# Kernel tuning notes

Measured on AMD Instinct MI355X. Metric: run time of the kernel, lower is better.

## Reference

```python
import jax, jax.numpy as jnp
import numpy as np

# bin sizes: logspace(-3,0,20) seconds, keep those < (t_end - t_start)/2 = 0.25 s, in ms
_bs = np.logspace(-3, 0, 20)
BIN_MS = [int(b) for b in np.round(_bs[_bs < 0.25] * 1000).astype(int)]  # 16 bins: [1,1,2,3,4,6,9,13,18,26,38,55,78,113,162,234]

SYNC_COST = 10.0
T_START_MS, T_END_MS = 0, 500
EPS = 1e-7


def setup_inputs() -> dict:
    C, B, T, N, N_E = 50, 8, 600, 30000, 24000
    rng = np.random.default_rng(42)
    spikes = (rng.random((B, T, N)) < 0.02).astype(np.float32)
    sample_trials = rng.integers(0, B, size=C).astype(np.int32)
    # sample_counts ~ N(70, 30) clipped to [15, N_E], consecutive chunks of a shuffled e-id list
    counts = np.clip(rng.normal(70.0, 30.0, C).astype(np.int64), 15, N_E)
    e_ids = rng.permutation(N_E)
    sel_mask = np.zeros((C, N), dtype=bool)
    prev = 0
    for i in range(C):
        cn = int(counts[i])
        if prev + cn > N_E:
            e_ids = rng.permutation(e_ids)
            prev = 0
        sel_mask[i, e_ids[prev:prev + cn]] = True
        prev += cn
    exp_fanos = (rng.random(len(BIN_MS)) * 1.5 + 0.5).astype(np.float32)
    return {
        "spikes": jnp.asarray(spikes),
        "exp_fanos": jnp.asarray(exp_fanos),
        "sample_trials": jnp.asarray(sample_trials),
        "sel_mask": jnp.asarray(sel_mask),
    }


def reference(spikes, exp_fanos, sample_trials, sel_mask):
    # trim to analysis window: [B, 500, N]
    sp = spikes[:, T_START_MS:T_END_MS, :]
    C = sel_mask.shape[0]
    m = sel_mask.astype(sp.dtype)  # [C, N]
    # population spike count per sample: sum over selected e-cells.
    # M[b, t, c] = sum_n sp[b,t,n] * m[c,n]; then pick the sampled trial per c.
    M = jnp.einsum('btn,cn->btc', sp, m)                 # [B, T, C] (small)
    selected = M[sample_trials, :, jnp.arange(C)]        # [C, T]
    T = selected.shape[1]
    fanos = []
    for b in BIN_MS:  # fixed small set of bin sizes
        nb = T // b
        # conv1d(ones, stride=b, VALID) == non-overlapping binned sums
        counts = selected[:, :nb * b].reshape(C, nb, b).sum(axis=-1)  # [C, nb]
        mean_count = jnp.maximum(counts.mean(axis=1), EPS)
        var_count = counts.var(axis=1)  # population variance, matches tf.math.reduce_variance
        fanos.append(jnp.mean(var_count / mean_count))
    fanos = jnp.stack(fanos)  # [16]
    mse_loss = jnp.mean(jnp.square(exp_fanos - fanos))
    return SYNC_COST * mse_loss
```

## Files before the change

### kernel.cpp

```cpp
#include <hip/hip_runtime.h>

#define C_CLS 50
#define B_TR 8
#define T_FULL 600
#define T_USE 500
#define N_NEU 30000
#define NGRP 118
#define NGRP_PAD 120
#define WPC 480
#define NQ 30
#define TPB 4
#define NBINS 16
#define EPS 1e-7
#define LDS_STRIDE 501

__device__ __constant__ int d_bins[NBINS] = {1,1,2,3,4,6,9,13,18,26,38,55,78,113,162,234};


__device__ __forceinline__ int mode_from_verdict(int v) {
    if (v & 1) return 2;
    if (v & 8) return 4;
    if (v & 2) return 1;
    if (v & 4) return 0;
    return 3;
}

__device__ __forceinline__ bool load_sel(const void* mask, int mode, long long e) {
    switch (mode) {
        case 0:  return ((const int*)mask)[e] != 0;
        case 1:  return ((const unsigned char*)mask)[e] != 0;
        case 2:  return ((const float*)mask)[e] != 0.0f;
        case 3:  return ((const long long*)mask)[e] != 0LL;
        default: return ((const double*)mask)[e] != 0.0;
    }
}

__global__ void __launch_bounds__(256)
detect_kernel(const unsigned int* __restrict__ w, const int* __restrict__ trials,
              int* verdict, int* ncls, int* cls_of_trial) {
    __shared__ int sfl;
    if (threadIdx.x == 0) sfl = 0;
    __syncthreads();
    const int nwords = C_CLS * N_NEU / 4;
    int per = (nwords + gridDim.x - 1) / gridDim.x;
    int beg = blockIdx.x * per;
    int end = beg + per; if (end > nwords) end = nwords;
    int f = 0;
    for (int i = beg + threadIdx.x; i < end; i += blockDim.x) {
        unsigned int v = w[i];
        if (v == 0u) continue;
        if (v == 0x3F800000u) f |= 1;
        else if (v == 0x3FF00000u && (i & 1)) f |= 8;
        else {
            unsigned int b0 = v & 0xFFu, b1 = (v >> 8) & 0xFFu,
                         b2 = (v >> 16) & 0xFFu, b3 = (v >> 24) & 0xFFu;
            bool byteOK = (b0 <= 1u) && (b1 <= 1u) && (b2 <= 1u) && (b3 <= 1u);
            if (byteOK && v != 1u) f |= 2;
        }
        if (i & 1) f |= 4;
    }
    if (f) atomicOr(&sfl, f);
    __syncthreads();
    if (threadIdx.x == 0) verdict[blockIdx.x] = sfl;

    if (blockIdx.x == 0 && threadIdx.x < 64) {
        int lane = threadIdx.x;
        int b = (lane < C_CLS) ? trials[lane] : -1;
        for (int bb = 0; bb < B_TR; ++bb) {
            unsigned long long m = __ballot(b == bb);
            if (b == bb) {
                int pos = __popcll(m & ((1ull << lane) - 1ull));
                cls_of_trial[bb * 64 + pos] = lane;
            }
            if (lane == 0) ncls[bb] = __popcll(m);
        }
    }
}

__global__ void build_bits_kernel(const void* mask, const int* __restrict__ verdict,
                                  unsigned long long* bits) {
    int c = blockIdx.x;
    int lane = threadIdx.x;
    int v = verdict[lane] | verdict[lane + 64] | verdict[lane + 128] | verdict[lane + 192];
    for (int off = 32; off > 0; off >>= 1) v |= __shfl_xor(v, off);
    int mode = mode_from_verdict(v);
    for (int g = blockIdx.y; g < NGRP_PAD; g += gridDim.y) {
        int base = g * 256 + lane * 4;
        long long e = (long long)c * N_NEU + base;
        bool s0 = (base + 0 < N_NEU) && load_sel(mask, mode, e + 0);
        bool s1 = (base + 1 < N_NEU) && load_sel(mask, mode, e + 1);
        bool s2 = (base + 2 < N_NEU) && load_sel(mask, mode, e + 2);
        bool s3 = (base + 3 < N_NEU) && load_sel(mask, mode, e + 3);
        unsigned long long w0 = __ballot(s0);
        unsigned long long w1 = __ballot(s1);
        unsigned long long w2 = __ballot(s2);
        unsigned long long w3 = __ballot(s3);
        if (lane == 0) {
            long long o = (long long)c * WPC + g * 4;
            bits[o + 0] = w0; bits[o + 1] = w1;
            bits[o + 2] = w2; bits[o + 3] = w3;
        }
    }
}

__global__ void __launch_bounds__(256)
stream_kernel(const float* __restrict__ spikes,
              const int* __restrict__ ncls,
              const int* __restrict__ cls_of_trial,
              const unsigned long long* __restrict__ bits,
              float* __restrict__ selected) {
    __shared__ unsigned long long sbits[TPB][WPC];
    __shared__ int wsum2[C_CLS][4][2];
    int bt = blockIdx.x;
    int b = bt / (T_USE / TPB);
    int tq = bt - b * (T_USE / TPB);
    int t0 = tq * TPB;
    int nc = ncls[b];
    if (nc == 0) return;
    int lane = threadIdx.x & 63;
    int wid = threadIdx.x >> 6;
    const float4* __restrict__ row4 =
        (const float4*)(spikes + ((long long)(b * T_FULL + t0 + wid)) * N_NEU);

    for (int q = 0; q < NQ; ++q) {
        float4 v[4];
#pragma unroll
        for (int u = 0; u < 4; ++u) {
            int ia = (q * 4 + u) * 64 + lane;
            if (ia > N_NEU / 4 - 1) ia = N_NEU / 4 - 1;
            v[u] = row4[ia];
        }
#pragma unroll
        for (int u = 0; u < 4; ++u) {
            unsigned long long b0 = __ballot(v[u].x != 0.0f);
            unsigned long long b1 = __ballot(v[u].y != 0.0f);
            unsigned long long b2 = __ballot(v[u].z != 0.0f);
            unsigned long long b3 = __ballot(v[u].w != 0.0f);
            if (lane == 0) {
                int o = (q * 4 + u) * 4;
                sbits[wid][o + 0] = b0; sbits[wid][o + 1] = b1;
                sbits[wid][o + 2] = b2; sbits[wid][o + 3] = b3;
            }
        }
    }
    __syncthreads();

    int i0 = threadIdx.x;
    int i1 = threadIdx.x + 256;
    bool has1 = (i1 < WPC);
    unsigned long long s00 = sbits[0][i0], s10 = sbits[1][i0],
                       s20 = sbits[2][i0], s30 = sbits[3][i0];
    unsigned long long s01 = 0, s11 = 0, s21 = 0, s31 = 0;
    if (has1) { s01 = sbits[0][i1]; s11 = sbits[1][i1];
                s21 = sbits[2][i1]; s31 = sbits[3][i1]; }
    for (int kc = 0; kc < nc; ++kc) {
        int c = cls_of_trial[b * 64 + kc];
        const unsigned long long* __restrict__ bp = bits + (long long)c * WPC;
        unsigned long long w0 = bp[i0];
        unsigned long long w1 = has1 ? bp[i1] : 0ull;
        int p0 = __popcll(s00 & w0) + __popcll(s01 & w1);
        int p1 = __popcll(s10 & w0) + __popcll(s11 & w1);
        int p2 = __popcll(s20 & w0) + __popcll(s21 & w1);
        int p3 = __popcll(s30 & w0) + __popcll(s31 & w1);
        int pa = p0 | (p1 << 16);
        int pb = p2 | (p3 << 16);
        for (int off = 32; off > 0; off >>= 1) {
            pa += __shfl_down(pa, off);
            pb += __shfl_down(pb, off);
        }
        if (lane == 0) { wsum2[kc][wid][0] = pa; wsum2[kc][wid][1] = pb; }
    }
    __syncthreads();
    if (threadIdx.x < nc * 4) {
        int kc = threadIdx.x >> 2, r = threadIdx.x & 3;
        int c = cls_of_trial[b * 64 + kc];
        int s = 0;
#pragma unroll
        for (int w = 0; w < 4; ++w) {
            int v = wsum2[kc][w][r >> 1];
            s += (r & 1) ? (v >> 16) : (v & 0xFFFF);
        }
        selected[c * T_USE + t0 + r] = (float)s;
    }
}

__global__ void __launch_bounds__(1024)
fano_loss_kernel(const float* __restrict__ selected,
                 const float* __restrict__ exp_fanos,
                 float* __restrict__ out) {
    __shared__ float lds[C_CLS * LDS_STRIDE];
    __shared__ float sf[NBINS];
    const float4* __restrict__ sel4 = (const float4*)selected;
    for (int i = threadIdx.x; i < C_CLS * T_USE / 4; i += 1024) {
        float4 v = sel4[i];
        int r = i / (T_USE / 4);
        int p = (i - r * (T_USE / 4)) * 4;
        float* dst = &lds[r * LDS_STRIDE + p];
        dst[0] = v.x; dst[1] = v.y; dst[2] = v.z; dst[3] = v.w;
    }
    __syncthreads();
    int wid = threadIdx.x >> 6;
    int lane = threadIdx.x & 63;
    int b = d_bins[wid];
    int nb = T_USE / b;
    float fano = 0.f;
    if (lane < C_CLS) {
        const float* row = &lds[lane * LDS_STRIDE];
        double s1 = 0.0, s2 = 0.0;
        for (int i = 0; i < nb; ++i) {
            float cs = 0.f;
            int base = i * b;
            for (int j = 0; j < b; ++j) cs += row[base + j];
            s1 += cs;
            s2 += (double)cs * (double)cs;
        }
        double mean = s1 / nb;
        double var = s2 / nb - mean * mean;
        if (var < 0.0) var = 0.0;
        double m = mean > EPS ? mean : EPS;
        fano = (float)(var / m);
    }
    for (int off = 32; off > 0; off >>= 1) fano += __shfl_down(fano, off);
    if (lane == 0) sf[wid] = fano / (float)C_CLS;
    __syncthreads();
    if (wid == 0) {
        float sq = 0.f;
        if (lane < NBINS) {
            float d = exp_fanos[lane] - sf[lane];
            sq = d * d;
        }
        for (int off = 32; off > 0; off >>= 1) sq += __shfl_down(sq, off);
        if (lane == 0) out[0] = 10.0f * sq / (float)NBINS;
    }
}

extern "C" void kernel_launch(void* const* d_in, const int* in_sizes, int n_in,
                              void* d_out, int out_size, void* d_ws, size_t ws_size,
                              hipStream_t stream) {
    const float* spikes    = (const float*)d_in[0];
    const float* exp_fanos = (const float*)d_in[1];
    const int*   trials    = (const int*)d_in[2];
    const void*  mask      = d_in[3];
    float* out = (float*)d_out;

    char* ws = (char*)d_ws;
    int*   verdict = (int*)(ws + 0);
    int*   ncls    = (int*)(ws + 1024);
    int*   clsofb  = (int*)(ws + 1280);
    unsigned long long* bits = (unsigned long long*)(ws + 8192);
    float* selected = (float*)(ws + 204800);

    detect_kernel<<<256, 256, 0, stream>>>((const unsigned int*)mask, trials,
                                           verdict, ncls, clsofb);
    build_bits_kernel<<<dim3(C_CLS, 8), 64, 0, stream>>>(mask, verdict, bits);
    stream_kernel<<<B_TR * (T_USE / TPB), 256, 0, stream>>>(spikes, ncls, clsofb,
                                                            bits, selected);
    fano_loss_kernel<<<1, 1024, 0, stream>>>(selected, exp_fanos, out);
}
```

Before: 181.3 us.

## Fuse four kernels into one cooperative persistent kernel with grid syncs

Replaces the detect, bit-build, streaming and fano kernels with one cooperative kernel of 512 blocks that separates phases with grid.sync. This removes three kernel launch gaps and the serial single-block fano stage. The fano stage is now split across 16 blocks, one per bin size, each reading rows straight from global memory instead of staging them in LDS. The cost is grid-wide barriers, a persistent loop over 1000 stream tiles in 512 blocks, and less parallelism in the bit-build phase.

```diff
diff --git a/kernel.cpp b/kernel.cpp
--- a/kernel.cpp
+++ b/kernel.cpp
@@ -1,4 +1,7 @@
 #include <hip/hip_runtime.h>
+#include <hip/hip_cooperative_groups.h>
+
+namespace cg = cooperative_groups;
 
 #define C_CLS 50
 #define B_TR 8
@@ -10,12 +13,12 @@
 #define WPC 480
 #define NQ 30
 #define TPB 4
+#define NBT (B_TR * T_USE / TPB)
+#define GRID 512
 #define NBINS 16
 #define EPS 1e-7
-#define LDS_STRIDE 501
 
 __device__ __constant__ int d_bins[NBINS] = {1,1,2,3,4,6,9,13,18,26,38,55,78,113,162,234};
-
 
 __device__ __forceinline__ int mode_from_verdict(int v) {
     if (v & 1) return 2;
@@ -35,198 +38,199 @@
     }
 }
 
-__global__ void __launch_bounds__(256)
-detect_kernel(const unsigned int* __restrict__ w, const int* __restrict__ trials,
-              int* verdict, int* ncls, int* cls_of_trial) {
-    __shared__ int sfl;
-    if (threadIdx.x == 0) sfl = 0;
-    __syncthreads();
-    const int nwords = C_CLS * N_NEU / 4;
-    int per = (nwords + gridDim.x - 1) / gridDim.x;
-    int beg = blockIdx.x * per;
-    int end = beg + per; if (end > nwords) end = nwords;
-    int f = 0;
-    for (int i = beg + threadIdx.x; i < end; i += blockDim.x) {
-        unsigned int v = w[i];
-        if (v == 0u) continue;
-        if (v == 0x3F800000u) f |= 1;
-        else if (v == 0x3FF00000u && (i & 1)) f |= 8;
-        else {
-            unsigned int b0 = v & 0xFFu, b1 = (v >> 8) & 0xFFu,
-                         b2 = (v >> 16) & 0xFFu, b3 = (v >> 24) & 0xFFu;
-            bool byteOK = (b0 <= 1u) && (b1 <= 1u) && (b2 <= 1u) && (b3 <= 1u);
-            if (byteOK && v != 1u) f |= 2;
-        }
-        if (i & 1) f |= 4;
-    }
-    if (f) atomicOr(&sfl, f);
-    __syncthreads();
-    if (threadIdx.x == 0) verdict[blockIdx.x] = sfl;
-
-    if (blockIdx.x == 0 && threadIdx.x < 64) {
-        int lane = threadIdx.x;
-        int b = (lane < C_CLS) ? trials[lane] : -1;
-        for (int bb = 0; bb < B_TR; ++bb) {
-            unsigned long long m = __ballot(b == bb);
-            if (b == bb) {
-                int pos = __popcll(m & ((1ull << lane) - 1ull));
-                cls_of_trial[bb * 64 + pos] = lane;
-            }
-            if (lane == 0) ncls[bb] = __popcll(m);
-        }
-    }
-}
-
-__global__ void build_bits_kernel(const void* mask, const int* __restrict__ verdict,
-                                  unsigned long long* bits) {
-    int c = blockIdx.x;
-    int lane = threadIdx.x;
-    int v = verdict[lane] | verdict[lane + 64] | verdict[lane + 128] | verdict[lane + 192];
-    for (int off = 32; off > 0; off >>= 1) v |= __shfl_xor(v, off);
-    int mode = mode_from_verdict(v);
-    for (int g = blockIdx.y; g < NGRP_PAD; g += gridDim.y) {
-        int base = g * 256 + lane * 4;
-        long long e = (long long)c * N_NEU + base;
-        bool s0 = (base + 0 < N_NEU) && load_sel(mask, mode, e + 0);
-        bool s1 = (base + 1 < N_NEU) && load_sel(mask, mode, e + 1);
-        bool s2 = (base + 2 < N_NEU) && load_sel(mask, mode, e + 2);
-        bool s3 = (base + 3 < N_NEU) && load_sel(mask, mode, e + 3);
-        unsigned long long w0 = __ballot(s0);
-        unsigned long long w1 = __ballot(s1);
-        unsigned long long w2 = __ballot(s2);
-        unsigned long long w3 = __ballot(s3);
-        if (lane == 0) {
-            long long o = (long long)c * WPC + g * 4;
-            bits[o + 0] = w0; bits[o + 1] = w1;
-            bits[o + 2] = w2; bits[o + 3] = w3;
-        }
-    }
-}
-
-__global__ void __launch_bounds__(256)
-stream_kernel(const float* __restrict__ spikes,
-              const int* __restrict__ ncls,
-              const int* __restrict__ cls_of_trial,
-              const unsigned long long* __restrict__ bits,
-              float* __restrict__ selected) {
+__global__ void __launch_bounds__(256, 2)
+fused_kernel(const float* __restrict__ spikes,
+             const float* __restrict__ exp_fanos,
+             const int* __restrict__ trials,
+             const void* __restrict__ mask,
+             float* __restrict__ out,
+             int* __restrict__ verdict,
+             int* __restrict__ ncls,
+             int* __restrict__ cls_of_trial,
+             unsigned long long* __restrict__ bits,
+             float* __restrict__ selected,
+             float* __restrict__ fanos) {
+    cg::grid_group grid = cg::this_grid();
     __shared__ unsigned long long sbits[TPB][WPC];
     __shared__ int wsum2[C_CLS][4][2];
-    int bt = blockIdx.x;
-    int b = bt / (T_USE / TPB);
-    int tq = bt - b * (T_USE / TPB);
-    int t0 = tq * TPB;
-    int nc = ncls[b];
-    if (nc == 0) return;
-    int lane = threadIdx.x & 63;
-    int wid = threadIdx.x >> 6;
-    const float4* __restrict__ row4 =
-        (const float4*)(spikes + ((long long)(b * T_FULL + t0 + wid)) * N_NEU);
-
-    for (int q = 0; q < NQ; ++q) {
-        float4 v[4];
-#pragma unroll
-        for (int u = 0; u < 4; ++u) {
-            int ia = (q * 4 + u) * 64 + lane;
-            if (ia > N_NEU / 4 - 1) ia = N_NEU / 4 - 1;
-            v[u] = row4[ia];
-        }
-#pragma unroll
-        for (int u = 0; u < 4; ++u) {
-            unsigned long long b0 = __ballot(v[u].x != 0.0f);
-            unsigned long long b1 = __ballot(v[u].y != 0.0f);
-            unsigned long long b2 = __ballot(v[u].z != 0.0f);
-            unsigned long long b3 = __ballot(v[u].w != 0.0f);
-            if (lane == 0) {
-                int o = (q * 4 + u) * 4;
-                sbits[wid][o + 0] = b0; sbits[wid][o + 1] = b1;
-                sbits[wid][o + 2] = b2; sbits[wid][o + 3] = b3;
-            }
-        }
-    }
-    __syncthreads();
-
-    int i0 = threadIdx.x;
-    int i1 = threadIdx.x + 256;
-    bool has1 = (i1 < WPC);
-    unsigned long long s00 = sbits[0][i0], s10 = sbits[1][i0],
-                       s20 = sbits[2][i0], s30 = sbits[3][i0];
-    unsigned long long s01 = 0, s11 = 0, s21 = 0, s31 = 0;
-    if (has1) { s01 = sbits[0][i1]; s11 = sbits[1][i1];
-                s21 = sbits[2][i1]; s31 = sbits[3][i1]; }
-    for (int kc = 0; kc < nc; ++kc) {
-        int c = cls_of_trial[b * 64 + kc];
-        const unsigned long long* __restrict__ bp = bits + (long long)c * WPC;
-        unsigned long long w0 = bp[i0];
-        unsigned long long w1 = has1 ? bp[i1] : 0ull;
-        int p0 = __popcll(s00 & w0) + __popcll(s01 & w1);
-        int p1 = __popcll(s10 & w0) + __popcll(s11 & w1);
-        int p2 = __popcll(s20 & w0) + __popcll(s21 & w1);
-        int p3 = __popcll(s30 & w0) + __popcll(s31 & w1);
-        int pa = p0 | (p1 << 16);
-        int pb = p2 | (p3 << 16);
-        for (int off = 32; off > 0; off >>= 1) {
-            pa += __shfl_down(pa, off);
-            pb += __shfl_down(pb, off);
-        }
-        if (lane == 0) { wsum2[kc][wid][0] = pa; wsum2[kc][wid][1] = pb; }
-    }
-    __syncthreads();
-    if (threadIdx.x < nc * 4) {
-        int kc = threadIdx.x >> 2, r = threadIdx.x & 3;
-        int c = cls_of_trial[b * 64 + kc];
-        int s = 0;
-#pragma unroll
-        for (int w = 0; w < 4; ++w) {
-            int v = wsum2[kc][w][r >> 1];
-            s += (r & 1) ? (v >> 16) : (v & 0xFFFF);
-        }
-        selected[c * T_USE + t0 + r] = (float)s;
-    }
-}
-
-__global__ void __launch_bounds__(1024)
-fano_loss_kernel(const float* __restrict__ selected,
-                 const float* __restrict__ exp_fanos,
-                 float* __restrict__ out) {
-    __shared__ float lds[C_CLS * LDS_STRIDE];
-    __shared__ float sf[NBINS];
-    const float4* __restrict__ sel4 = (const float4*)selected;
-    for (int i = threadIdx.x; i < C_CLS * T_USE / 4; i += 1024) {
-        float4 v = sel4[i];
-        int r = i / (T_USE / 4);
-        int p = (i - r * (T_USE / 4)) * 4;
-        float* dst = &lds[r * LDS_STRIDE + p];
-        dst[0] = v.x; dst[1] = v.y; dst[2] = v.z; dst[3] = v.w;
-    }
-    __syncthreads();
-    int wid = threadIdx.x >> 6;
-    int lane = threadIdx.x & 63;
-    int b = d_bins[wid];
-    int nb = T_USE / b;
-    float fano = 0.f;
-    if (lane < C_CLS) {
-        const float* row = &lds[lane * LDS_STRIDE];
-        double s1 = 0.0, s2 = 0.0;
-        for (int i = 0; i < nb; ++i) {
+    __shared__ int sfl;
+
+    const int bid = blockIdx.x;
+    const int tid = threadIdx.x;
+    const int lane = tid & 63;
+    const int wid = tid >> 6;
+
+    {
+        if (tid == 0) sfl = 0;
+        __syncthreads();
+        const unsigned int* w = (const unsigned int*)mask;
+        const int nwords = C_CLS * N_NEU / 4;
+        int f = 0;
+        for (int i = bid * 256 + tid; i < nwords; i += GRID * 256) {
+            unsigned int v = w[i];
+            if (v == 0u) continue;
+            if (v == 0x3F800000u) f |= 1;
+            else if (v == 0x3FF00000u && (i & 1)) f |= 8;
+            else {
+                unsigned int b0 = v & 0xFFu, b1 = (v >> 8) & 0xFFu,
+                             b2 = (v >> 16) & 0xFFu, b3 = (v >> 24) & 0xFFu;
+                bool byteOK = (b0 <= 1u) && (b1 <= 1u) && (b2 <= 1u) && (b3 <= 1u);
+                if (byteOK && v != 1u) f |= 2;
+            }
+            if (i & 1) f |= 4;
+        }
+        for (int off = 32; off > 0; off >>= 1) f |= __shfl_xor(f, off);
+        if (lane == 0 && f) atomicOr(&sfl, f);
+        __syncthreads();
+        if (tid == 0) verdict[bid] = sfl;
+
+        if (bid == 0 && tid < 64) {
+            int b = (lane < C_CLS) ? trials[lane] : -1;
+            for (int bb = 0; bb < B_TR; ++bb) {
+                unsigned long long m = __ballot(b == bb);
+                if (b == bb) {
+                    int pos = __popcll(m & ((1ull << lane) - 1ull));
+                    cls_of_trial[bb * 64 + pos] = lane;
+                }
+                if (lane == 0) ncls[bb] = __popcll(m);
+            }
+        }
+    }
+    __threadfence();
+    grid.sync();
+
+    {
+        if (tid == 0) sfl = 0;
+        __syncthreads();
+        int v = verdict[tid] | verdict[tid + 256];
+        for (int off = 32; off > 0; off >>= 1) v |= __shfl_xor(v, off);
+        if (lane == 0 && v) atomicOr(&sfl, v);
+        __syncthreads();
+        int mode = mode_from_verdict(sfl);
+        for (int task = bid; task < C_CLS * NGRP_PAD; task += GRID) {
+            int c = task / NGRP_PAD;
+            int g = task - c * NGRP_PAD;
+            int n = g * 256 + lane * 4 + wid;
+            bool sel = (n < N_NEU) && load_sel(mask, mode, (long long)c * N_NEU + n);
+            unsigned long long w = __ballot(sel);
+            if (lane == 0) bits[(long long)c * WPC + g * 4 + wid] = w;
+        }
+    }
+    __threadfence();
+    grid.sync();
+
+    for (int bt = bid; bt < NBT; bt += GRID) {
+        int b = bt / (T_USE / TPB);
+        int tq = bt - b * (T_USE / TPB);
+        int t0 = tq * TPB;
+        int nc = ncls[b];
+        if (nc == 0) continue;
+        const float4* __restrict__ row4 =
+            (const float4*)(spikes + ((long long)(b * T_FULL + t0 + wid)) * N_NEU);
+
+        for (int q = 0; q < NQ; ++q) {
+            float4 v[4];
+#pragma unroll
+            for (int u = 0; u < 4; ++u) {
+                int ia = (q * 4 + u) * 64 + lane;
+                if (ia > N_NEU / 4 - 1) ia = N_NEU / 4 - 1;
+                v[u] = row4[ia];
+            }
+#pragma unroll
+            for (int u = 0; u < 4; ++u) {
+                unsigned long long b0 = __ballot(v[u].x != 0.0f);
+                unsigned long long b1 = __ballot(v[u].y != 0.0f);
+                unsigned long long b2 = __ballot(v[u].z != 0.0f);
+                unsigned long long b3 = __ballot(v[u].w != 0.0f);
+                if (lane == 0) {
+                    int o = (q * 4 + u) * 4;
+                    sbits[wid][o + 0] = b0; sbits[wid][o + 1] = b1;
+                    sbits[wid][o + 2] = b2; sbits[wid][o + 3] = b3;
+                }
+            }
+        }
+        __syncthreads();
+
+        int i0 = tid;
+        int i1 = tid + 256;
+        bool has1 = (i1 < WPC);
+        unsigned long long s00 = sbits[0][i0], s10 = sbits[1][i0],
+                           s20 = sbits[2][i0], s30 = sbits[3][i0];
+        unsigned long long s01 = 0, s11 = 0, s21 = 0, s31 = 0;
+        if (has1) { s01 = sbits[0][i1]; s11 = sbits[1][i1];
+                    s21 = sbits[2][i1]; s31 = sbits[3][i1]; }
+        for (int kc = 0; kc < nc; ++kc) {
+            int c = cls_of_trial[b * 64 + kc];
+            const unsigned long long* __restrict__ bp = bits + (long long)c * WPC;
+            unsigned long long w0 = bp[i0];
+            unsigned long long w1 = has1 ? bp[i1] : 0ull;
+            int p0 = __popcll(s00 & w0) + __popcll(s01 & w1);
+            int p1 = __popcll(s10 & w0) + __popcll(s11 & w1);
+            int p2 = __popcll(s20 & w0) + __popcll(s21 & w1);
+            int p3 = __popcll(s30 & w0) + __popcll(s31 & w1);
+            int pa = p0 | (p1 << 16);
+            int pb = p2 | (p3 << 16);
+            for (int off = 32; off > 0; off >>= 1) {
+                pa += __shfl_down(pa, off);
+                pb += __shfl_down(pb, off);
+            }
+            if (lane == 0) { wsum2[kc][wid][0] = pa; wsum2[kc][wid][1] = pb; }
+        }
+        __syncthreads();
+        if (tid < nc * 4) {
+            int kc = tid >> 2, r = tid & 3;
+            int c = cls_of_trial[b * 64 + kc];
+            int s = 0;
+#pragma unroll
+            for (int w = 0; w < 4; ++w) {
+                int v = wsum2[kc][w][r >> 1];
+                s += (r & 1) ? (v >> 16) : (v & 0xFFFF);
+            }
+            selected[c * T_USE + t0 + r] = (float)s;
+        }
+    }
+    __threadfence();
+    grid.sync();
+
+    if (bid < NBINS && tid < 64) {
+        int b = d_bins[bid];
+        int nb = T_USE / b;
+        int lim = nb * b;
+        float fano = 0.f;
+        if (lane < C_CLS) {
+            const float4* __restrict__ row4 = (const float4*)(selected + lane * T_USE);
+            double s1 = 0.0, s2 = 0.0;
             float cs = 0.f;
-            int base = i * b;
-            for (int j = 0; j < b; ++j) cs += row[base + j];
-            s1 += cs;
-            s2 += (double)cs * (double)cs;
-        }
-        double mean = s1 / nb;
-        double var = s2 / nb - mean * mean;
-        if (var < 0.0) var = 0.0;
-        double m = mean > EPS ? mean : EPS;
-        fano = (float)(var / m);
-    }
-    for (int off = 32; off > 0; off >>= 1) fano += __shfl_down(fano, off);
-    if (lane == 0) sf[wid] = fano / (float)C_CLS;
-    __syncthreads();
-    if (wid == 0) {
+            int r = b;
+            for (int i4 = 0; i4 < T_USE / 4; ++i4) {
+                float4 v = row4[i4];
+                float comp0 = v.x, comp1 = v.y, comp2 = v.z, comp3 = v.w;
+#pragma unroll
+                for (int u = 0; u < 4; ++u) {
+                    float cv = (u == 0) ? comp0 : (u == 1) ? comp1 : (u == 2) ? comp2 : comp3;
+                    int idx = i4 * 4 + u;
+                    if (idx < lim) {
+                        cs += cv;
+                        if (--r == 0) { s1 += cs; s2 += (double)cs * cs; cs = 0.f; r = b; }
+                    }
+                }
+            }
+            double mean = s1 / nb;
+            double var = s2 / nb - mean * mean;
+            if (var < 0.0) var = 0.0;
+            double m = mean > EPS ? mean : EPS;
+            fano = (float)(var / m);
+        }
+        for (int off = 32; off > 0; off >>= 1) fano += __shfl_down(fano, off);
+        if (lane == 0) fanos[bid] = fano / (float)C_CLS;
+    }
+    __threadfence();
+    grid.sync();
+
+    if (bid == 0 && tid < 64) {
         float sq = 0.f;
         if (lane < NBINS) {
-            float d = exp_fanos[lane] - sf[lane];
+            float d = exp_fanos[lane] - fanos[lane];
             sq = d * d;
         }
         for (int off = 32; off > 0; off >>= 1) sq += __shfl_down(sq, off);
@@ -245,15 +249,17 @@
 
     char* ws = (char*)d_ws;
     int*   verdict = (int*)(ws + 0);
-    int*   ncls    = (int*)(ws + 1024);
-    int*   clsofb  = (int*)(ws + 1280);
+    int*   ncls    = (int*)(ws + 2048);
+    int*   clsofb  = (int*)(ws + 2304);
+    float* fanos   = (float*)(ws + 4608);
     unsigned long long* bits = (unsigned long long*)(ws + 8192);
     float* selected = (float*)(ws + 204800);
 
-    detect_kernel<<<256, 256, 0, stream>>>((const unsigned int*)mask, trials,
-                                           verdict, ncls, clsofb);
-    build_bits_kernel<<<dim3(C_CLS, 8), 64, 0, stream>>>(mask, verdict, bits);
-    stream_kernel<<<B_TR * (T_USE / TPB), 256, 0, stream>>>(spikes, ncls, clsofb,
-                                                            bits, selected);
-    fano_loss_kernel<<<1, 1024, 0, stream>>>(selected, exp_fanos, out);
-}
+    void* args[] = {
+        (void*)&spikes, (void*)&exp_fanos, (void*)&trials, (void*)&mask,
+        (void*)&out, (void*)&verdict, (void*)&ncls, (void*)&clsofb,
+        (void*)&bits, (void*)&selected, (void*)&fanos
+    };
+    hipLaunchCooperativeKernel((void*)fused_kernel, dim3(GRID), dim3(256),
+                               args, 0, stream);
+}
```

Result: slower. 483.3 us (+166.6%).

## Split spike rows across two waves per timestep and software-pipeline loads

Applied to the files above, without the earlier changes.

The stream kernel now handles 2 timesteps per block instead of 4, with two waves splitting each 30000-neuron row in half. This doubles the block count for more parallelism. Each wave double-buffers its float4 loads so the next chunk's global reads are issued before the ballots on the current one. The bitmask words are padded to 512 per class, which removes the tail guards, and launch bounds ask for 4 blocks per CU. The risks are extra register pressure from the prefetch buffers and the need for build_bits and the bits workspace to agree with the new 512-word padding.

```diff
diff --git a/kernel.cpp b/kernel.cpp
--- a/kernel.cpp
+++ b/kernel.cpp
@@ -5,11 +5,12 @@
 #define T_FULL 600
 #define T_USE 500
 #define N_NEU 30000
-#define NGRP 118
-#define NGRP_PAD 120
-#define WPC 480
-#define NQ 30
-#define TPB 4
+#define NF4 7500
+#define NGRP_PAD 128
+#define WPC 512
+#define NQHALF 16
+#define TPB 2
+#define NBT (B_TR * T_USE / TPB)
 #define NBINS 16
 #define EPS 1e-7
 #define LDS_STRIDE 501
@@ -103,14 +104,40 @@
     }
 }
 
-__global__ void __launch_bounds__(256)
+__device__ __forceinline__ void loadq(float4* v, const float4* __restrict__ row4,
+                                      int qq, int lane) {
+#pragma unroll
+    for (int u = 0; u < 4; ++u) {
+        int ia = (qq * 4 + u) * 64 + lane;
+        if (ia > NF4 - 1) ia = NF4 - 1;
+        v[u] = row4[ia];
+    }
+}
+
+__device__ __forceinline__ void consumeq(const float4* v, unsigned long long* sb,
+                                         int qq, int lane) {
+#pragma unroll
+    for (int u = 0; u < 4; ++u) {
+        unsigned long long b0 = __ballot(v[u].x != 0.0f);
+        unsigned long long b1 = __ballot(v[u].y != 0.0f);
+        unsigned long long b2 = __ballot(v[u].z != 0.0f);
+        unsigned long long b3 = __ballot(v[u].w != 0.0f);
+        if (lane == 0) {
+            int o = (qq * 4 + u) * 4;
+            sb[o + 0] = b0; sb[o + 1] = b1;
+            sb[o + 2] = b2; sb[o + 3] = b3;
+        }
+    }
+}
+
+__global__ void __launch_bounds__(256, 4)
 stream_kernel(const float* __restrict__ spikes,
               const int* __restrict__ ncls,
               const int* __restrict__ cls_of_trial,
               const unsigned long long* __restrict__ bits,
               float* __restrict__ selected) {
     __shared__ unsigned long long sbits[TPB][WPC];
-    __shared__ int wsum2[C_CLS][4][2];
+    __shared__ int wsum[C_CLS][4];
     int bt = blockIdx.x;
     int b = bt / (T_USE / TPB);
     int tq = bt - b * (T_USE / TPB);
@@ -119,68 +146,56 @@
     if (nc == 0) return;
     int lane = threadIdx.x & 63;
     int wid = threadIdx.x >> 6;
+    int r = wid >> 1;
+    int h = wid & 1;
     const float4* __restrict__ row4 =
-        (const float4*)(spikes + ((long long)(b * T_FULL + t0 + wid)) * N_NEU);
-
-    for (int q = 0; q < NQ; ++q) {
-        float4 v[4];
-#pragma unroll
-        for (int u = 0; u < 4; ++u) {
-            int ia = (q * 4 + u) * 64 + lane;
-            if (ia > N_NEU / 4 - 1) ia = N_NEU / 4 - 1;
-            v[u] = row4[ia];
-        }
-#pragma unroll
-        for (int u = 0; u < 4; ++u) {
-            unsigned long long b0 = __ballot(v[u].x != 0.0f);
-            unsigned long long b1 = __ballot(v[u].y != 0.0f);
-            unsigned long long b2 = __ballot(v[u].z != 0.0f);
-            unsigned long long b3 = __ballot(v[u].w != 0.0f);
-            if (lane == 0) {
-                int o = (q * 4 + u) * 4;
-                sbits[wid][o + 0] = b0; sbits[wid][o + 1] = b1;
-                sbits[wid][o + 2] = b2; sbits[wid][o + 3] = b3;
-            }
+        (const float4*)(spikes + ((long long)(b * T_FULL + t0 + r)) * N_NEU);
+
+    int qb = h * NQHALF;
+    float4 A[4], B[4], NA[4], NB[4];
+    loadq(A, row4, qb + 0, lane);
+    loadq(B, row4, qb + 1, lane);
+    for (int q = 0; q < NQHALF; q += 2) {
+        bool more = (q + 2 < NQHALF);
+        if (more) {
+            loadq(NA, row4, qb + q + 2, lane);
+            loadq(NB, row4, qb + q + 3, lane);
+        }
+        consumeq(A, sbits[r], qb + q, lane);
+        consumeq(B, sbits[r], qb + q + 1, lane);
+        if (more) {
+#pragma unroll
+            for (int u = 0; u < 4; ++u) { A[u] = NA[u]; B[u] = NB[u]; }
         }
     }
     __syncthreads();
 
     int i0 = threadIdx.x;
     int i1 = threadIdx.x + 256;
-    bool has1 = (i1 < WPC);
-    unsigned long long s00 = sbits[0][i0], s10 = sbits[1][i0],
-                       s20 = sbits[2][i0], s30 = sbits[3][i0];
-    unsigned long long s01 = 0, s11 = 0, s21 = 0, s31 = 0;
-    if (has1) { s01 = sbits[0][i1]; s11 = sbits[1][i1];
-                s21 = sbits[2][i1]; s31 = sbits[3][i1]; }
+    unsigned long long s00 = sbits[0][i0], s01 = sbits[0][i1];
+    unsigned long long s10 = sbits[1][i0], s11 = sbits[1][i1];
     for (int kc = 0; kc < nc; ++kc) {
         int c = cls_of_trial[b * 64 + kc];
         const unsigned long long* __restrict__ bp = bits + (long long)c * WPC;
         unsigned long long w0 = bp[i0];
-        unsigned long long w1 = has1 ? bp[i1] : 0ull;
+        unsigned long long w1 = bp[i1];
         int p0 = __popcll(s00 & w0) + __popcll(s01 & w1);
         int p1 = __popcll(s10 & w0) + __popcll(s11 & w1);
-        int p2 = __popcll(s20 & w0) + __popcll(s21 & w1);
-        int p3 = __popcll(s30 & w0) + __popcll(s31 & w1);
         int pa = p0 | (p1 << 16);
-        int pb = p2 | (p3 << 16);
-        for (int off = 32; off > 0; off >>= 1) {
-            pa += __shfl_down(pa, off);
-            pb += __shfl_down(pb, off);
-        }
-        if (lane == 0) { wsum2[kc][wid][0] = pa; wsum2[kc][wid][1] = pb; }
-    }
-    __syncthreads();
-    if (threadIdx.x < nc * 4) {
-        int kc = threadIdx.x >> 2, r = threadIdx.x & 3;
+        for (int off = 32; off > 0; off >>= 1) pa += __shfl_down(pa, off);
+        if (lane == 0) wsum[kc][wid] = pa;
+    }
+    __syncthreads();
+    if (threadIdx.x < nc * 2) {
+        int kc = threadIdx.x >> 1, rr = threadIdx.x & 1;
         int c = cls_of_trial[b * 64 + kc];
         int s = 0;
 #pragma unroll
         for (int w = 0; w < 4; ++w) {
-            int v = wsum2[kc][w][r >> 1];
-            s += (r & 1) ? (v >> 16) : (v & 0xFFFF);
-        }
-        selected[c * T_USE + t0 + r] = (float)s;
+            int v = wsum[kc][w];
+            s += rr ? (v >> 16) : (v & 0xFFFF);
+        }
+        selected[c * T_USE + t0 + rr] = (float)s;
     }
 }
 
@@ -248,12 +263,11 @@
     int*   ncls    = (int*)(ws + 1024);
     int*   clsofb  = (int*)(ws + 1280);
     unsigned long long* bits = (unsigned long long*)(ws + 8192);
-    float* selected = (float*)(ws + 204800);
+    float* selected = (float*)(ws + 212992);
 
     detect_kernel<<<256, 256, 0, stream>>>((const unsigned int*)mask, trials,
                                            verdict, ncls, clsofb);
     build_bits_kernel<<<dim3(C_CLS, 8), 64, 0, stream>>>(mask, verdict, bits);
-    stream_kernel<<<B_TR * (T_USE / TPB), 256, 0, stream>>>(spikes, ncls, clsofb,
-                                                            bits, selected);
+    stream_kernel<<<NBT, 256, 0, stream>>>(spikes, ncls, clsofb, bits, selected);
     fano_loss_kernel<<<1, 1024, 0, stream>>>(selected, exp_fanos, out);
 }
```

New measurement: 183.2 us. Within noise of the previous version (+1.0%).
